# Optimization experiments

Measured on AMD Instinct MI355X. Metric: run time of the kernel, lower is better.

## Reference

```python
import jax, jax.numpy as jnp
import numpy as np

CHUNK = 512  # query-point chunk size; per-chunk intermediate is CHUNK x M x 3


def _min_sqdist(a, b):
    """For each point in a [N,3], min over b [M,3] of squared Euclidean distance.
    Chunked over a to avoid materializing the full NxM matrix (mirrors KDTree's
    avoidance of the dense matrix)."""
    n = a.shape[0]
    a_chunks = a.reshape(n // CHUNK, CHUNK, a.shape[1])

    def body(carry, ac):
        # ac: [CHUNK,3]; d: [CHUNK,M]
        d = jnp.sum((ac[:, None, :] - b[None, :, :]) ** 2, axis=-1)
        return carry, jnp.min(d, axis=1)

    _, mins = jax.lax.scan(body, None, a_chunks)
    return mins.reshape(n)


def setup_inputs() -> dict:
    key = jax.random.key(0)
    k1, k2 = jax.random.split(key)
    gt_points = jax.random.normal(k1, (16384, 3), dtype=jnp.float32)
    gen_points = jax.random.normal(k2, (16384, 3), dtype=jnp.float32)
    return {"gt_points": gt_points, "gen_points": gen_points}


def reference(gt_points, gen_points):
    # KDTree.query returns Euclidean distance; original squares then means,
    # which equals mean of squared nearest-neighbor distances.
    gt_to_gen = jnp.mean(_min_sqdist(gt_points, gen_points))
    gen_to_gt = jnp.mean(_min_sqdist(gen_points, gt_points))
    return gt_to_gen + gen_to_gt
```

## Files before the change

### kernel.cpp

```cpp
#include <hip/hip_runtime.h>
#include <float.h>


#define NPTS 16384
constexpr int QPB   = 64;
constexpr int NBLK  = NPTS / QPB;
constexpr int NFRAG = NPTS / 32;
constexpr int FPW   = NFRAG / 8;
constexpr int SET_SHORTS = NFRAG * 512;

typedef float f32x16 __attribute__((ext_vector_type(16)));
typedef short bf16x8 __attribute__((ext_vector_type(8)));

__device__ inline ushort bf16rne(float f) {
    uint u = __float_as_uint(f);
    u += 0x7fff + ((u >> 16) & 1);
    return (ushort)(u >> 16);
}
__device__ inline float bf2f(ushort h) { return __uint_as_float(((uint)h) << 16); }

__global__ __launch_bounds__(512) void cd_prep(const float* __restrict__ gt,
                                               const float* __restrict__ gen,
                                               short* __restrict__ bt,
                                               float* __restrict__ out) {
    if (blockIdx.x == 0 && threadIdx.x == 0) out[0] = 0.0f;

    const int t   = blockIdx.x * 512 + threadIdx.x;
    const int set = t >> 15;
    const int rem = t & 32767;
    const int h   = rem >> 14;
    const int p   = rem & (NPTS - 1);
    const float* __restrict__ src = set ? gen : gt;

    const float x = src[3 * p + 0], y = src[3 * p + 1], z = src[3 * p + 2];
    const ushort hx = bf16rne(x), hy = bf16rne(y), hz = bf16rne(z);
    const ushort lx = bf16rne(x - bf2f(hx));
    const ushort ly = bf16rne(y - bf2f(hy));
    const ushort lz = bf16rne(z - bf2f(hz));
    const float w = fmaf(x, x, fmaf(y, y, z * z));
    const ushort wh = bf16rne(w), wl = bf16rne(w - bf2f(wh));

    bf16x8 v;
    if (h == 0)
        v = (bf16x8){(short)hx, (short)hy, (short)hz, (short)hx,
                     (short)hy, (short)hz, (short)lx, (short)ly};
    else
        v = (bf16x8){(short)lz, (short)lx, (short)ly, (short)lz,
                     (short)wh, (short)wl, (short)0, (short)0};
    *(bf16x8*)(bt + set * SET_SHORTS + (p >> 5) * 512 + (h * 32 + (p & 31)) * 8) = v;
}

__global__ __launch_bounds__(512, 4) void cd_main(const float* __restrict__ gt,
                                                  const float* __restrict__ gen,
                                                  const short* __restrict__ bt,
                                                  float* __restrict__ out) {
    const int dir = blockIdx.y;
    const float* __restrict__ Q = dir ? gen : gt;
    const short* __restrict__ BT = bt + (dir ? 0 : SET_SHORTS);

    __shared__ float wm[8][QPB];

    const int tid  = threadIdx.x;
    const int lane = tid & 63;
    const int wave = __builtin_amdgcn_readfirstlane(tid >> 6);

    const int arow = lane & 31, kg = lane >> 5;
    const int qbase = blockIdx.x * QPB;
    bf16x8 a[2];
    #pragma unroll
    for (int f = 0; f < 2; ++f) {
        const int q = qbase + f * 32 + arow;
        const float x = Q[3 * q + 0], y = Q[3 * q + 1], z = Q[3 * q + 2];
        const float ux = -2.f * x, uy = -2.f * y, uz = -2.f * z;
        const ushort hx = bf16rne(ux), hy = bf16rne(uy), hz = bf16rne(uz);
        const ushort lx = bf16rne(ux - bf2f(hx));
        const ushort ly = bf16rne(uy - bf2f(hy));
        const ushort lz = bf16rne(uz - bf2f(hz));
        if (kg == 0)
            a[f] = (bf16x8){(short)hx, (short)hy, (short)hz, (short)lx,
                            (short)ly, (short)lz, (short)hx, (short)hy};
        else
            a[f] = (bf16x8){(short)hz, (short)lx, (short)ly, (short)lz,
                            (short)0x3f80, (short)0x3f80, (short)0, (short)0};
    }

    f32x16 mm0 = (f32x16)(FLT_MAX), mm1 = (f32x16)(FLT_MAX);
    const f32x16 zc = (f32x16)(0.f);

    const short* rb = BT + (wave * FPW) * 512 + lane * 8;
    bf16x8 b0 = *(const bf16x8*)(rb);
    bf16x8 b1 = *(const bf16x8*)(rb + 512);
    for (int f2 = 0; f2 < FPW; f2 += 2) {
        const int nf = (f2 + 2) & (FPW - 1);
        const bf16x8 n0 = *(const bf16x8*)(rb + nf * 512);
        const bf16x8 n1 = *(const bf16x8*)(rb + (nf + 1) * 512);
        const f32x16 d00 = __builtin_amdgcn_mfma_f32_32x32x16_bf16(a[0], b0, zc, 0, 0, 0);
        const f32x16 d01 = __builtin_amdgcn_mfma_f32_32x32x16_bf16(a[0], b1, zc, 0, 0, 0);
        #pragma unroll
        for (int i = 0; i < 16; ++i)
            mm0[i] = fminf(fminf(d00[i], d01[i]), mm0[i]);
        const f32x16 d10 = __builtin_amdgcn_mfma_f32_32x32x16_bf16(a[1], b0, zc, 0, 0, 0);
        const f32x16 d11 = __builtin_amdgcn_mfma_f32_32x32x16_bf16(a[1], b1, zc, 0, 0, 0);
        #pragma unroll
        for (int i = 0; i < 16; ++i)
            mm1[i] = fminf(fminf(d10[i], d11[i]), mm1[i]);
        b0 = n0; b1 = n1;
    }

    #pragma unroll
    for (int i = 0; i < 16; ++i) {
        float v0 = mm0[i], v1 = mm1[i];
        #pragma unroll
        for (int off = 1; off <= 16; off <<= 1) {
            v0 = fminf(v0, __shfl_xor(v0, off, 64));
            v1 = fminf(v1, __shfl_xor(v1, off, 64));
        }
        const int row = (i & 3) + 8 * (i >> 2) + 4 * kg;
        if ((lane & 31) == 0) {
            wm[wave][row]      = v0;
            wm[wave][32 + row] = v1;
        }
    }
    __syncthreads();

    if (tid < QPB) {
        float v = wm[0][tid];
        #pragma unroll
        for (int w = 1; w < 8; ++w) v = fminf(v, wm[w][tid]);
        const int q = qbase + tid;
        const float x = Q[3 * q + 0], y = Q[3 * q + 1], z = Q[3 * q + 2];
        v += fmaf(x, x, fmaf(y, y, z * z));
        #pragma unroll
        for (int off = 32; off > 0; off >>= 1) v += __shfl_down(v, off, 64);
        if (tid == 0) atomicAdd(out, v * (1.0f / (float)NPTS));
    }
}

extern "C" void kernel_launch(void* const* d_in, const int* in_sizes, int n_in,
                              void* d_out, int out_size, void* d_ws, size_t ws_size,
                              hipStream_t stream) {
    const float* gt  = (const float*)d_in[0];
    const float* gen = (const float*)d_in[1];
    short* bt        = (short*)d_ws;
    float* out       = (float*)d_out;

    cd_prep<<<128, 512, 0, stream>>>(gt, gen, bt, out);
    dim3 grid(NBLK, 2);
    cd_main<<<grid, 512, 0, stream>>>(gt, gen, bt, out);
}
```

Measured before the change: 82.88 us.

## Double queries per block to reuse each loaded B fragment across four A fragments

Raises queries per block from 64 to 128, so each wave holds four A fragments and reuses every loaded pair of reference fragments for eight MFMAs instead of four. This halves the number of blocks and the total global/L2 traffic for the reference set. The software prefetch of the next B fragments is removed in favour of plain in-loop loads, and launch bounds are lowered to 2 blocks per CU to make room for the extra accumulator registers. The final atomic now fires once per wave for the 128-query tail. Risks are lower occupancy, exposed load latency without the explicit prefetch, and only 256 blocks in the grid.

New measurement: 90.66 us. 1.09x slower.

```diff
diff --git a/kernel.cpp b/kernel.cpp
--- a/kernel.cpp
+++ b/kernel.cpp
@@ -3,7 +3,8 @@
 
 
 #define NPTS 16384
-constexpr int QPB   = 64;
+constexpr int QPB   = 128;
+constexpr int NAF   = 4;
 constexpr int NBLK  = NPTS / QPB;
 constexpr int NFRAG = NPTS / 32;
 constexpr int FPW   = NFRAG / 8;
@@ -50,7 +51,7 @@
     *(bf16x8*)(bt + set * SET_SHORTS + (p >> 5) * 512 + (h * 32 + (p & 31)) * 8) = v;
 }
 
-__global__ __launch_bounds__(512, 4) void cd_main(const float* __restrict__ gt,
+__global__ __launch_bounds__(512, 2) void cd_main(const float* __restrict__ gt,
                                                   const float* __restrict__ gen,
                                                   const short* __restrict__ bt,
                                                   float* __restrict__ out) {
@@ -66,9 +67,9 @@
 
     const int arow = lane & 31, kg = lane >> 5;
     const int qbase = blockIdx.x * QPB;
-    bf16x8 a[2];
+    bf16x8 a[NAF];
     #pragma unroll
-    for (int f = 0; f < 2; ++f) {
+    for (int f = 0; f < NAF; ++f) {
         const int q = qbase + f * 32 + arow;
         const float x = Q[3 * q + 0], y = Q[3 * q + 1], z = Q[3 * q + 2];
         const float ux = -2.f * x, uy = -2.f * y, uz = -2.f * z;
@@ -84,41 +85,35 @@
                             (short)0x3f80, (short)0x3f80, (short)0, (short)0};
     }
 
-    f32x16 mm0 = (f32x16)(FLT_MAX), mm1 = (f32x16)(FLT_MAX);
+    f32x16 mm[NAF];
+    #pragma unroll
+    for (int f = 0; f < NAF; ++f) mm[f] = (f32x16)(FLT_MAX);
     const f32x16 zc = (f32x16)(0.f);
 
     const short* rb = BT + (wave * FPW) * 512 + lane * 8;
-    bf16x8 b0 = *(const bf16x8*)(rb);
-    bf16x8 b1 = *(const bf16x8*)(rb + 512);
     for (int f2 = 0; f2 < FPW; f2 += 2) {
-        const int nf = (f2 + 2) & (FPW - 1);
-        const bf16x8 n0 = *(const bf16x8*)(rb + nf * 512);
-        const bf16x8 n1 = *(const bf16x8*)(rb + (nf + 1) * 512);
-        const f32x16 d00 = __builtin_amdgcn_mfma_f32_32x32x16_bf16(a[0], b0, zc, 0, 0, 0);
-        const f32x16 d01 = __builtin_amdgcn_mfma_f32_32x32x16_bf16(a[0], b1, zc, 0, 0, 0);
+        const bf16x8 b0 = *(const bf16x8*)(rb + f2 * 512);
+        const bf16x8 b1 = *(const bf16x8*)(rb + (f2 + 1) * 512);
         #pragma unroll
-        for (int i = 0; i < 16; ++i)
-            mm0[i] = fminf(fminf(d00[i], d01[i]), mm0[i]);
-        const f32x16 d10 = __builtin_amdgcn_mfma_f32_32x32x16_bf16(a[1], b0, zc, 0, 0, 0);
-        const f32x16 d11 = __builtin_amdgcn_mfma_f32_32x32x16_bf16(a[1], b1, zc, 0, 0, 0);
-        #pragma unroll
-        for (int i = 0; i < 16; ++i)
-            mm1[i] = fminf(fminf(d10[i], d11[i]), mm1[i]);
-        b0 = n0; b1 = n1;
+        for (int f = 0; f < NAF; ++f) {
+            const f32x16 d0 = __builtin_amdgcn_mfma_f32_32x32x16_bf16(a[f], b0, zc, 0, 0, 0);
+            const f32x16 d1 = __builtin_amdgcn_mfma_f32_32x32x16_bf16(a[f], b1, zc, 0, 0, 0);
+            #pragma unroll
+            for (int i = 0; i < 16; ++i)
+                mm[f][i] = fminf(fminf(d0[i], d1[i]), mm[f][i]);
+        }
     }
 
     #pragma unroll
-    for (int i = 0; i < 16; ++i) {
-        float v0 = mm0[i], v1 = mm1[i];
+    for (int f = 0; f < NAF; ++f) {
         #pragma unroll
-        for (int off = 1; off <= 16; off <<= 1) {
-            v0 = fminf(v0, __shfl_xor(v0, off, 64));
-            v1 = fminf(v1, __shfl_xor(v1, off, 64));
-        }
-        const int row = (i & 3) + 8 * (i >> 2) + 4 * kg;
-        if ((lane & 31) == 0) {
-            wm[wave][row]      = v0;
-            wm[wave][32 + row] = v1;
+        for (int i = 0; i < 16; ++i) {
+            float v = mm[f][i];
+            #pragma unroll
+            for (int off = 1; off <= 16; off <<= 1)
+                v = fminf(v, __shfl_xor(v, off, 64));
+            const int row = (i & 3) + 8 * (i >> 2) + 4 * kg;
+            if ((lane & 31) == 0) wm[wave][f * 32 + row] = v;
         }
     }
     __syncthreads();
@@ -132,7 +127,7 @@
         v += fmaf(x, x, fmaf(y, y, z * z));
         #pragma unroll
         for (int off = 32; off > 0; off >>= 1) v += __shfl_down(v, off, 64);
-        if (tid == 0) atomicAdd(out, v * (1.0f / (float)NPTS));
+        if ((tid & 63) == 0) atomicAdd(out, v * (1.0f / (float)NPTS));
     }
 }
 
```
